# Optimization experiments

Hardware: AMD Instinct MI355X
Metric: run time of the kernel (lower is better)

Reference implementation:

```python
import jax, jax.numpy as jnp
import numpy as np

EMBED_SIZE = 1024
HEADS = 16
HEAD_DIM = EMBED_SIZE // HEADS
NEG_INF = -1e20


def setup_inputs() -> dict:
    key = jax.random.key(0)
    k1, k2, k3, k4, k5, k6, k7 = jax.random.split(key, 7)
    N, S = 2, 2048
    values = jax.random.normal(k1, (N, S, EMBED_SIZE), dtype=jnp.float32)
    keys = jax.random.normal(k2, (N, S, EMBED_SIZE), dtype=jnp.float32)
    query = jax.random.normal(k3, (N, S, EMBED_SIZE), dtype=jnp.float32)
    mask = jnp.ones((N, 1, S, S), dtype=bool)
    # Per-head projection weights (shared across heads), torch Linear convention y = x @ W.T
    sc = 1.0 / np.sqrt(HEAD_DIM)
    Wq = jax.random.uniform(k4, (HEAD_DIM, HEAD_DIM), jnp.float32, -sc, sc)
    Wk = jax.random.uniform(k5, (HEAD_DIM, HEAD_DIM), jnp.float32, -sc, sc)
    Wv = jax.random.uniform(k6, (HEAD_DIM, HEAD_DIM), jnp.float32, -sc, sc)
    sco = 1.0 / np.sqrt(EMBED_SIZE)
    k7a, k7b = jax.random.split(k7)
    Wo = jax.random.uniform(k7a, (EMBED_SIZE, EMBED_SIZE), jnp.float32, -sco, sco)
    bo = jax.random.uniform(k7b, (EMBED_SIZE,), jnp.float32, -sco, sco)
    return {"values": values, "keys": keys, "query": query, "mask": mask,
            "Wq": Wq, "Wk": Wk, "Wv": Wv, "Wo": Wo, "bo": bo}


def reference(values, keys, query, mask, Wq, Wk, Wv, Wo, bo):
    N, Q, E = query.shape
    K = keys.shape[1]
    H, D = HEADS, HEAD_DIM
    v = values.reshape(N, K, H, D)
    k = keys.reshape(N, K, H, D)
    q = query.reshape(N, Q, H, D)
    # per-head linear (weights shared across heads): y = x @ W.T
    q = jnp.einsum('nqhd,ed->nqhe', q, Wq)
    k = jnp.einsum('nkhd,ed->nkhe', k, Wk)
    v = jnp.einsum('nkhd,ed->nkhe', v, Wv)
    energy = jnp.einsum('nqhd,nkhd->nhqk', q, k)  # [N,H,Q,K]
    energy = jnp.where(mask, energy, NEG_INF)
    # NOTE: original scales by sqrt(embed_size), not sqrt(head_dim)
    attn = jax.nn.softmax(energy / (E ** 0.5), axis=-1)
    out = jnp.einsum('nhqk,nkhd->nqhd', attn, v).reshape(N, Q, H * D)
    return out @ Wo.T + bo
```

## Files before the change

kernel.cpp:

```cpp
#include <hip/hip_runtime.h>
#include <hip/hip_bf16.h>


typedef __bf16 bf16_t;
typedef __bf16 bf16x4_t __attribute__((ext_vector_type(4)));
typedef __bf16 bf16x8_t __attribute__((ext_vector_type(8)));
typedef float f32x4_t __attribute__((ext_vector_type(4)));

#define MFMA16(a, b, c) __builtin_amdgcn_mfma_f32_16x16x32_bf16((a), (b), (c), 0, 0, 0)

static __device__ __forceinline__ bf16x8_t cvt8(float4 a, float4 b) {
  bf16x8_t r = { (bf16_t)a.x, (bf16_t)a.y, (bf16_t)a.z, (bf16_t)a.w,
                 (bf16_t)b.x, (bf16_t)b.y, (bf16_t)b.z, (bf16_t)b.w };
  return r;
}

__global__ __launch_bounds__(256) void k_cvt_wo(const float* __restrict__ w,
                                                bf16_t* __restrict__ o) {
  int i = (blockIdx.x * 256 + threadIdx.x) * 4;
  float4 v = *(const float4*)(w + i);
  bf16x4_t r = { (bf16_t)v.x, (bf16_t)v.y, (bf16_t)v.z, (bf16_t)v.w };
  *(bf16x4_t*)(o + i) = r;
}

__global__ __launch_bounds__(256) void k_tilemask(const int* __restrict__ mask32,
                                                  unsigned char* __restrict__ tm) {
  const int b = blockIdx.x;
  const int n = b >> 10, qt = (b >> 5) & 31, kt = b & 31;
  const int t = threadIdx.x;
  const int row = t >> 2;
  const int mtype = (mask32[0] == 1);
  bool ok;
  if (mtype) {
    const uint4* base = (const uint4*)(mask32 + (size_t)n * 4194304 +
                                       (size_t)(qt * 64 + row) * 2048 + kt * 64);
    ok = true;
    #pragma unroll
    for (int j = 0; j < 4; ++j) {
      uint4 v = base[(t & 3) * 4 + j];
      ok = ok && v.x && v.y && v.z && v.w;
    }
  } else {
    const unsigned char* maskb = (const unsigned char*)mask32;
    const int c = (t & 3) * 16;
    uint4 v = *(const uint4*)(maskb + (size_t)n * 4194304 +
                              (size_t)(qt * 64 + row) * 2048 + kt * 64 + c);
    ok = ((v.x & v.y & v.z & v.w) == 0x01010101u);
  }
  __shared__ int ok_s;
  if (t == 0) ok_s = 1;
  __syncthreads();
  if (!ok) atomicAnd(&ok_s, 0);
  __syncthreads();
  if (t == 0) tm[b] = (unsigned char)ok_s;
}

__global__ __launch_bounds__(256) void k_proj_qk(const float* __restrict__ x,
                                                 const float* __restrict__ w,
                                                 bf16_t* __restrict__ out, float oscale) {
  __shared__ __align__(16) ushort Xs[256 * 64];
  const int t = threadIdx.x;
  const int r0 = blockIdx.x * 256;
  const int lane = t & 63, wv = t >> 6;
  const int g = lane >> 4, l15 = lane & 15;
  #pragma unroll
  for (int i = 0; i < 16; ++i) {
    int c = t + 256 * i;
    float4 v = *(const float4*)(x + (size_t)r0 * 64 + (size_t)c * 4);
    int row = c >> 4;
    int off = ((c & 15) * 8) ^ ((row & 7) << 4);
    bf16x4_t bv = { (bf16_t)v.x, (bf16_t)v.y, (bf16_t)v.z, (bf16_t)v.w };
    *(bf16x4_t*)((char*)Xs + row * 128 + off) = bv;
  }
  bf16x8_t bw[4][2];
  #pragma unroll
  for (int nf = 0; nf < 4; ++nf)
    #pragma unroll
    for (int ks = 0; ks < 2; ++ks) {
      const float* wp = w + (nf * 16 + l15) * 64 + ks * 32 + g * 8;
      bw[nf][ks] = cvt8(*(const float4*)wp, *(const float4*)(wp + 4));
    }
  __syncthreads();
  f32x4_t acc[4][4] = {};
  #pragma unroll
  for (int mi = 0; mi < 4; ++mi) {
    int row = wv * 64 + mi * 16 + l15;
    int sw = (row & 7) << 4;
    bf16x8_t a0 = *(const bf16x8_t*)((char*)Xs + row * 128 + ((g * 16) ^ sw));
    bf16x8_t a1 = *(const bf16x8_t*)((char*)Xs + row * 128 + ((64 + g * 16) ^ sw));
    #pragma unroll
    for (int nf = 0; nf < 4; ++nf) {
      acc[mi][nf] = MFMA16(a0, bw[nf][0], acc[mi][nf]);
      acc[mi][nf] = MFMA16(a1, bw[nf][1], acc[mi][nf]);
    }
  }
  #pragma unroll
  for (int mi = 0; mi < 4; ++mi)
    #pragma unroll
    for (int rr = 0; rr < 4; ++rr) {
      int r = r0 + wv * 64 + mi * 16 + g * 4 + rr;
      int h = r & 15, s = (r >> 4) & 2047, n = r >> 15;
      bf16_t* op = out + ((size_t)(n * 16 + h) * 2048 + s) * 64;
      #pragma unroll
      for (int nf = 0; nf < 4; ++nf)
        op[nf * 16 + l15] = (bf16_t)(acc[mi][nf][rr] * oscale);
    }
}

__global__ __launch_bounds__(256) void k_proj_v(const float* __restrict__ x,
                                                const float* __restrict__ w,
                                                bf16_t* __restrict__ vt) {
  const int b = blockIdx.x;
  const int sb = b & 7, nh = b >> 3;
  const int h = nh & 15, n = nh >> 4;
  const int t = threadIdx.x, lane = t & 63, wv = t >> 6;
  const int g = lane >> 4, l15 = lane & 15;
  const int s0 = sb * 256 + wv * 64;
  bf16x8_t bx[4][2];
  #pragma unroll
  for (int ni = 0; ni < 4; ++ni)
    #pragma unroll
    for (int ks = 0; ks < 2; ++ks) {
      int s = s0 + ni * 16 + l15;
      const float* xp = x + ((size_t)n * 2048 + s) * 1024 + h * 64 + ks * 32 + g * 8;
      bx[ni][ks] = cvt8(*(const float4*)xp, *(const float4*)(xp + 4));
    }
  f32x4_t acc[4][4] = {};
  #pragma unroll
  for (int mi = 0; mi < 4; ++mi) {
    const float* wp = w + (mi * 16 + l15) * 64 + g * 8;
    bf16x8_t a0 = cvt8(*(const float4*)wp, *(const float4*)(wp + 4));
    bf16x8_t a1 = cvt8(*(const float4*)(wp + 32), *(const float4*)(wp + 36));
    #pragma unroll
    for (int ni = 0; ni < 4; ++ni) {
      acc[mi][ni] = MFMA16(a0, bx[ni][0], acc[mi][ni]);
      acc[mi][ni] = MFMA16(a1, bx[ni][1], acc[mi][ni]);
    }
  }
  #pragma unroll
  for (int mi = 0; mi < 4; ++mi)
    #pragma unroll
    for (int rr = 0; rr < 4; ++rr) {
      int d = mi * 16 + g * 4 + rr;
      bf16_t* vp = vt + ((size_t)nh * 64 + d) * 2048 + s0;
      #pragma unroll
      for (int ni = 0; ni < 4; ++ni)
        vp[ni * 16 + l15] = (bf16_t)acc[mi][ni][rr];
    }
}

__global__ __launch_bounds__(256) void k_attn(const bf16_t* __restrict__ Qp,
                                              const bf16_t* __restrict__ Kp,
                                              const bf16_t* __restrict__ VT,
                                              const int* __restrict__ mask32,
                                              const unsigned char* __restrict__ tm,
                                              bf16_t* __restrict__ ao) {
  __shared__ __align__(16) ushort Ks[64 * 64];
  __shared__ __align__(16) ushort Vs[64 * 64];
  __shared__ __align__(16) ushort Ps[4 * 32 * 64];
  const int b = blockIdx.x;
  const int qb = b & 15, nh = b >> 4;
  const int n = nh >> 4, h = nh & 15;
  const int t = threadIdx.x, lane = t & 63, wv = t >> 6;
  const int g = lane >> 4, l15 = lane & 15;
  const int q0 = qb * 128 + wv * 32;
  const size_t kvbase = (size_t)nh * (2048 * 64);
  const int mtype = (mask32[0] == 1);

  bf16x8_t aq[2][2];
  #pragma unroll
  for (int mi = 0; mi < 2; ++mi)
    #pragma unroll
    for (int ks = 0; ks < 2; ++ks) {
      int qrow = q0 + mi * 16 + l15;
      aq[mi][ks] = *(const bf16x8_t*)(Qp + kvbase + (size_t)qrow * 64 + ks * 32 + g * 8);
    }

  f32x4_t o[2][4] = {};
  float mrow[2][4], lrow[2][4];
  #pragma unroll
  for (int mi = 0; mi < 2; ++mi)
    #pragma unroll
    for (int rr = 0; rr < 4; ++rr) { mrow[mi][rr] = -__builtin_inff(); lrow[mi][rr] = 0.f; }

  const unsigned char* tmrow = tm + ((size_t)n * 32 + (q0 >> 6)) * 32;
  const int srow = t >> 2, sc = t & 3;
  const int ssw = (srow & 7) << 4;

  for (int kt = 0; kt < 32; ++kt) {
    const int kb = kt * 64;
    {
      const float4* gk = (const float4*)(Kp + kvbase + (size_t)kb * 64);
      float4 k0 = gk[t * 2], k1 = gk[t * 2 + 1];
      *(float4*)((char*)Ks + srow * 128 + ((sc * 32) ^ ssw)) = k0;
      *(float4*)((char*)Ks + srow * 128 + ((sc * 32 + 16) ^ ssw)) = k1;
      const bf16_t* gv = VT + kvbase + (size_t)srow * 2048 + kb + sc * 16;
      float4 v0 = *(const float4*)gv, v1 = *(const float4*)(gv + 8);
      *(float4*)((char*)Vs + srow * 128 + ((sc * 32) ^ ssw)) = v0;
      *(float4*)((char*)Vs + srow * 128 + ((sc * 32 + 16) ^ ssw)) = v1;
    }
    __syncthreads();
    f32x4_t sfr[2][4] = {};
    #pragma unroll
    for (int ks = 0; ks < 2; ++ks)
      #pragma unroll
      for (int nf = 0; nf < 4; ++nf) {
        int kr = nf * 16 + l15;
        bf16x8_t kf = *(const bf16x8_t*)((char*)Ks + kr * 128 + ((ks * 64 + g * 16) ^ ((kr & 7) << 4)));
        sfr[0][nf] = MFMA16(aq[0][ks], kf, sfr[0][nf]);
        sfr[1][nf] = MFMA16(aq[1][ks], kf, sfr[1][nf]);
      }
    if (!tmrow[kt]) {
      #pragma unroll
      for (int mi = 0; mi < 2; ++mi)
        #pragma unroll
        for (int nf = 0; nf < 4; ++nf)
          #pragma unroll
          for (int rr = 0; rr < 4; ++rr) {
            int qrow = q0 + mi * 16 + g * 4 + rr;
            int kcol = kb + nf * 16 + l15;
            size_t mi_idx = (size_t)n * 4194304 + (size_t)qrow * 2048 + kcol;
            bool mv = mtype ? (mask32[mi_idx] != 0)
                            : (((const unsigned char*)mask32)[mi_idx] != 0);
            if (!mv) sfr[mi][nf][rr] = -3.125e18f;
          }
    }
    #pragma unroll
    for (int mi = 0; mi < 2; ++mi) {
      float al[4];
      #pragma unroll
      for (int rr = 0; rr < 4; ++rr) {
        float mx = fmaxf(fmaxf(sfr[mi][0][rr], sfr[mi][1][rr]),
                         fmaxf(sfr[mi][2][rr], sfr[mi][3][rr]));
        mx = fmaxf(mx, __shfl_xor(mx, 1));
        mx = fmaxf(mx, __shfl_xor(mx, 2));
        mx = fmaxf(mx, __shfl_xor(mx, 4));
        mx = fmaxf(mx, __shfl_xor(mx, 8));
        float mn = fmaxf(mrow[mi][rr], mx);
        al[rr] = __expf(mrow[mi][rr] - mn);
        mrow[mi][rr] = mn;
        float rs = 0.f;
        #pragma unroll
        for (int nf = 0; nf < 4; ++nf) {
          float p = __expf(sfr[mi][nf][rr] - mn);
          sfr[mi][nf][rr] = p;
          rs += p;
        }
        rs += __shfl_xor(rs, 1); rs += __shfl_xor(rs, 2);
        rs += __shfl_xor(rs, 4); rs += __shfl_xor(rs, 8);
        lrow[mi][rr] = lrow[mi][rr] * al[rr] + rs;
      }
      #pragma unroll
      for (int df = 0; df < 4; ++df)
        #pragma unroll
        for (int rr = 0; rr < 4; ++rr)
          o[mi][df][rr] *= al[rr];
      #pragma unroll
      for (int rr = 0; rr < 4; ++rr) {
        int prow = wv * 32 + mi * 16 + g * 4 + rr;
        char* pp = (char*)Ps + prow * 128;
        int sw = (prow & 7) << 4;
        #pragma unroll
        for (int nf = 0; nf < 4; ++nf)
          *(bf16_t*)(pp + (((nf * 16 + l15) * 2) ^ sw)) = (bf16_t)sfr[mi][nf][rr];
      }
    }
    asm volatile("" ::: "memory");
    #pragma unroll
    for (int ks = 0; ks < 2; ++ks) {
      bf16x8_t pa[2];
      #pragma unroll
      for (int mi = 0; mi < 2; ++mi) {
        int prow = wv * 32 + mi * 16 + l15;
        pa[mi] = *(const bf16x8_t*)((char*)Ps + prow * 128 + ((ks * 64 + g * 16) ^ ((prow & 7) << 4)));
      }
      #pragma unroll
      for (int df = 0; df < 4; ++df) {
        int vr = df * 16 + l15;
        bf16x8_t vf = *(const bf16x8_t*)((char*)Vs + vr * 128 + ((ks * 64 + g * 16) ^ ((vr & 7) << 4)));
        o[0][df] = MFMA16(pa[0], vf, o[0][df]);
        o[1][df] = MFMA16(pa[1], vf, o[1][df]);
      }
    }
    __syncthreads();
  }
  #pragma unroll
  for (int mi = 0; mi < 2; ++mi)
    #pragma unroll
    for (int rr = 0; rr < 4; ++rr) {
      float inv = 1.f / lrow[mi][rr];
      int qrow = q0 + mi * 16 + g * 4 + rr;
      bf16_t* op = ao + ((size_t)n * 2048 + qrow) * 1024 + h * 64;
      #pragma unroll
      for (int df = 0; df < 4; ++df)
        op[df * 16 + l15] = (bf16_t)(o[mi][df][rr] * inv);
    }
}

__global__ __launch_bounds__(256) void k_gemm_out(const bf16_t* __restrict__ A,
                                                  const bf16_t* __restrict__ B,
                                                  const float* __restrict__ bias,
                                                  float* __restrict__ C) {
  __shared__ __align__(16) ushort As[128 * 32];
  __shared__ __align__(16) ushort Bs[128 * 32];
  const int bx = blockIdx.x;
  const int mb = bx >> 3, nb = bx & 7;
  const int m0 = mb * 128, n0 = nb * 128;
  const int t = threadIdx.x, lane = t & 63, wv = t >> 6;
  const int g = lane >> 4, l15 = lane & 15;
  const int wm = (wv >> 1) * 64, wn = (wv & 1) * 64;
  const int srow = t >> 1, sc = (t & 1) * 16;
  f32x4_t acc[4][4] = {};
  for (int k0 = 0; k0 < 1024; k0 += 32) {
    float4 a0 = *(const float4*)(A + (size_t)(m0 + srow) * 1024 + k0 + sc);
    float4 a1 = *(const float4*)(A + (size_t)(m0 + srow) * 1024 + k0 + sc + 8);
    float4 b0 = *(const float4*)(B + (size_t)(n0 + srow) * 1024 + k0 + sc);
    float4 b1 = *(const float4*)(B + (size_t)(n0 + srow) * 1024 + k0 + sc + 8);
    *(float4*)((char*)As + srow * 64 + sc * 2) = a0;
    *(float4*)((char*)As + srow * 64 + sc * 2 + 16) = a1;
    *(float4*)((char*)Bs + srow * 64 + sc * 2) = b0;
    *(float4*)((char*)Bs + srow * 64 + sc * 2 + 16) = b1;
    __syncthreads();
    bf16x8_t af[4], bfr[4];
    #pragma unroll
    for (int mi = 0; mi < 4; ++mi)
      af[mi] = *(const bf16x8_t*)((char*)As + (wm + mi * 16 + l15) * 64 + g * 16);
    #pragma unroll
    for (int ni = 0; ni < 4; ++ni)
      bfr[ni] = *(const bf16x8_t*)((char*)Bs + (wn + ni * 16 + l15) * 64 + g * 16);
    #pragma unroll
    for (int mi = 0; mi < 4; ++mi)
      #pragma unroll
      for (int ni = 0; ni < 4; ++ni)
        acc[mi][ni] = MFMA16(af[mi], bfr[ni], acc[mi][ni]);
    __syncthreads();
  }
  float bv[4];
  #pragma unroll
  for (int ni = 0; ni < 4; ++ni) bv[ni] = bias[n0 + wn + ni * 16 + l15];
  #pragma unroll
  for (int mi = 0; mi < 4; ++mi)
    #pragma unroll
    for (int rr = 0; rr < 4; ++rr) {
      int row = m0 + wm + mi * 16 + g * 4 + rr;
      float* cp = C + (size_t)row * 1024 + n0 + wn;
      #pragma unroll
      for (int ni = 0; ni < 4; ++ni)
        cp[ni * 16 + l15] = acc[mi][ni][rr] + bv[ni];
    }
}

extern "C" void kernel_launch(void* const* d_in, const int* in_sizes, int n_in,
                              void* d_out, int out_size, void* d_ws, size_t ws_size,
                              hipStream_t stream) {
  (void)in_sizes; (void)n_in; (void)out_size; (void)ws_size;
  const float* values = (const float*)d_in[0];
  const float* keys   = (const float*)d_in[1];
  const float* query  = (const float*)d_in[2];
  const int*   mask   = (const int*)d_in[3];
  const float* Wq = (const float*)d_in[4];
  const float* Wk = (const float*)d_in[5];
  const float* Wv = (const float*)d_in[6];
  const float* Wo = (const float*)d_in[7];
  const float* bo = (const float*)d_in[8];
  float* out = (float*)d_out;

  char* ws = (char*)d_ws;
  bf16_t* Qp  = (bf16_t*)(ws);
  bf16_t* Kp  = (bf16_t*)(ws + (8u << 20));
  bf16_t* VTp = (bf16_t*)(ws + (16u << 20));
  bf16_t* AO  = (bf16_t*)(ws + (24u << 20));
  bf16_t* WOb = (bf16_t*)(ws + (32u << 20));
  unsigned char* TM = (unsigned char*)(ws + (34u << 20));

  k_cvt_wo<<<dim3(1024), dim3(256), 0, stream>>>(Wo, WOb);
  k_tilemask<<<dim3(2048), dim3(256), 0, stream>>>(mask, TM);
  k_proj_qk<<<dim3(256), dim3(256), 0, stream>>>(query, Wq, Qp, 0.03125f);
  k_proj_qk<<<dim3(256), dim3(256), 0, stream>>>(keys, Wk, Kp, 1.0f);
  k_proj_v<<<dim3(256), dim3(256), 0, stream>>>(values, Wv, VTp);
  k_attn<<<dim3(512), dim3(256), 0, stream>>>(Qp, Kp, VTp, mask, TM, AO);
  k_gemm_out<<<dim3(256), dim3(256), 0, stream>>>(AO, WOb, bo, out);
}
```

Baseline: 304.7 us.

## Rewrite attention kernel with 32x32 MFMA, transposed scores, and double-buffered LDS loads

The attention kernel now computes S^T with 32x32x16 MFMAs, so each lane owns one query row. That makes the row max and sum a single cross-half shuffle, and P can be rebuilt into the PV operand in registers instead of going through shared memory. K/V tiles are double-buffered and loaded straight into LDS with global_load_lds, overlapping the next tile's load with compute. Blocks grow to 512 threads covering 256 queries on half as many blocks, which may reduce parallelism across the GPU's CUs and raises register pressure.

```diff
diff --git a/kernel.cpp b/kernel.cpp
--- a/kernel.cpp
+++ b/kernel.cpp
@@ -6,13 +6,21 @@
 typedef __bf16 bf16x4_t __attribute__((ext_vector_type(4)));
 typedef __bf16 bf16x8_t __attribute__((ext_vector_type(8)));
 typedef float f32x4_t __attribute__((ext_vector_type(4)));
+typedef float f32x16_t __attribute__((ext_vector_type(16)));
 
 #define MFMA16(a, b, c) __builtin_amdgcn_mfma_f32_16x16x32_bf16((a), (b), (c), 0, 0, 0)
+#define MFMA32(a, b, c) __builtin_amdgcn_mfma_f32_32x32x16_bf16((a), (b), (c), 0, 0, 0)
 
 static __device__ __forceinline__ bf16x8_t cvt8(float4 a, float4 b) {
   bf16x8_t r = { (bf16_t)a.x, (bf16_t)a.y, (bf16_t)a.z, (bf16_t)a.w,
                  (bf16_t)b.x, (bf16_t)b.y, (bf16_t)b.z, (bf16_t)b.w };
   return r;
+}
+
+static __device__ __forceinline__ unsigned pack2(float a, float b) {
+  union { bf16_t h[2]; unsigned u; } x;
+  x.h[0] = (bf16_t)a; x.h[1] = (bf16_t)b;
+  return x.u;
 }
 
 __global__ __launch_bounds__(256) void k_cvt_wo(const float* __restrict__ w,
@@ -149,152 +157,157 @@
     }
 }
 
-__global__ __launch_bounds__(256) void k_attn(const bf16_t* __restrict__ Qp,
-                                              const bf16_t* __restrict__ Kp,
-                                              const bf16_t* __restrict__ VT,
-                                              const int* __restrict__ mask32,
-                                              const unsigned char* __restrict__ tm,
-                                              bf16_t* __restrict__ ao) {
-  __shared__ __align__(16) ushort Ks[64 * 64];
-  __shared__ __align__(16) ushort Vs[64 * 64];
-  __shared__ __align__(16) ushort Ps[4 * 32 * 64];
+__global__ __launch_bounds__(512, 2) void k_attn(const bf16_t* __restrict__ Qp,
+                                                 const bf16_t* __restrict__ Kp,
+                                                 const bf16_t* __restrict__ VT,
+                                                 const int* __restrict__ mask32,
+                                                 const unsigned char* __restrict__ tm,
+                                                 bf16_t* __restrict__ ao) {
+  __shared__ __align__(128) char lds[32768];
   const int b = blockIdx.x;
-  const int qb = b & 15, nh = b >> 4;
+  const int qb = b & 7, nh = b >> 3;
   const int n = nh >> 4, h = nh & 15;
   const int t = threadIdx.x, lane = t & 63, wv = t >> 6;
-  const int g = lane >> 4, l15 = lane & 15;
-  const int q0 = qb * 128 + wv * 32;
+  const int l31 = lane & 31, hi = lane >> 5;
+  const int q0w = qb * 256 + wv * 32;
   const size_t kvbase = (size_t)nh * (2048 * 64);
   const int mtype = (mask32[0] == 1);
 
-  bf16x8_t aq[2][2];
-  #pragma unroll
-  for (int mi = 0; mi < 2; ++mi)
-    #pragma unroll
-    for (int ks = 0; ks < 2; ++ks) {
-      int qrow = q0 + mi * 16 + l15;
-      aq[mi][ks] = *(const bf16x8_t*)(Qp + kvbase + (size_t)qrow * 64 + ks * 32 + g * 8);
-    }
-
-  f32x4_t o[2][4] = {};
-  float mrow[2][4], lrow[2][4];
-  #pragma unroll
-  for (int mi = 0; mi < 2; ++mi)
-    #pragma unroll
-    for (int rr = 0; rr < 4; ++rr) { mrow[mi][rr] = -__builtin_inff(); lrow[mi][rr] = 0.f; }
-
-  const unsigned char* tmrow = tm + ((size_t)n * 32 + (q0 >> 6)) * 32;
-  const int srow = t >> 2, sc = t & 3;
-  const int ssw = (srow & 7) << 4;
+  bf16x8_t qf[4];
+  #pragma unroll
+  for (int kd = 0; kd < 4; ++kd)
+    qf[kd] = *(const bf16x8_t*)(Qp + kvbase + (size_t)(q0w + l31) * 64 + kd * 16 + hi * 8);
+
+  f32x16_t o0 = {}, o1 = {};
+  float m_r = -3.0e38f, l_r = 0.f;
+
+  const unsigned char* tmrow = tm + ((size_t)n * 32 + (q0w >> 6)) * 32;
+
+  const int srow = lane >> 3, schunk = lane & 7;
+  const int soff = ((schunk << 4) ^ (srow << 4));
+  const char* gK = (const char*)(Kp + kvbase);
+  const char* gV = (const char*)(VT + kvbase);
+
+#define STAGE(ktile, bufsel)                                                          \
+  do {                                                                                \
+    const int kb_ = (ktile) * 64;                                                     \
+    char* ldsK_ = lds + (bufsel) * 16384 + wv * 1024;                                 \
+    char* ldsV_ = lds + (bufsel) * 16384 + 8192 + wv * 1024;                          \
+    __builtin_amdgcn_global_load_lds(                                                 \
+        (const __attribute__((address_space(1))) void*)(gK + (size_t)(kb_ + wv * 8 + srow) * 128 + soff), \
+        (__attribute__((address_space(3))) void*)ldsK_, 16, 0, 0);                    \
+    __builtin_amdgcn_global_load_lds(                                                 \
+        (const __attribute__((address_space(1))) void*)(gV + (size_t)(wv * 8 + srow) * 4096 + (size_t)kb_ * 2 + soff), \
+        (__attribute__((address_space(3))) void*)ldsV_, 16, 0, 0);                    \
+  } while (0)
+
+  int buf = 0;
+  STAGE(0, 0);
+  asm volatile("s_waitcnt vmcnt(0)" ::: "memory");
+  __syncthreads();
 
   for (int kt = 0; kt < 32; ++kt) {
-    const int kb = kt * 64;
-    {
-      const float4* gk = (const float4*)(Kp + kvbase + (size_t)kb * 64);
-      float4 k0 = gk[t * 2], k1 = gk[t * 2 + 1];
-      *(float4*)((char*)Ks + srow * 128 + ((sc * 32) ^ ssw)) = k0;
-      *(float4*)((char*)Ks + srow * 128 + ((sc * 32 + 16) ^ ssw)) = k1;
-      const bf16_t* gv = VT + kvbase + (size_t)srow * 2048 + kb + sc * 16;
-      float4 v0 = *(const float4*)gv, v1 = *(const float4*)(gv + 8);
-      *(float4*)((char*)Vs + srow * 128 + ((sc * 32) ^ ssw)) = v0;
-      *(float4*)((char*)Vs + srow * 128 + ((sc * 32 + 16) ^ ssw)) = v1;
-    }
+    if (kt < 31) STAGE(kt + 1, buf ^ 1);
+    const char* Ksb = lds + buf * 16384;
+    const char* Vsb = Ksb + 8192;
+    const int rsw = (l31 & 7) << 4;
+
+    f32x16_t s0 = {}, s1 = {};
+    #pragma unroll
+    for (int kd = 0; kd < 4; ++kd) {
+      int off = kd * 32 + hi * 16;
+      bf16x8_t k0 = *(const bf16x8_t*)(Ksb + l31 * 128 + (off ^ rsw));
+      bf16x8_t k1 = *(const bf16x8_t*)(Ksb + (32 + l31) * 128 + (off ^ rsw));
+      s0 = MFMA32(k0, qf[kd], s0);
+      s1 = MFMA32(k1, qf[kd], s1);
+    }
+
+    if (!tmrow[kt]) {
+      #pragma unroll
+      for (int r = 0; r < 16; ++r) {
+        int krow = (r & 3) + 8 * (r >> 2) + 4 * hi;
+        size_t base = (size_t)n * 4194304 + (size_t)(q0w + l31) * 2048 + kt * 64 + krow;
+        bool m0 = mtype ? (mask32[base] != 0) : (((const unsigned char*)mask32)[base] != 0);
+        bool m1 = mtype ? (mask32[base + 32] != 0) : (((const unsigned char*)mask32)[base + 32] != 0);
+        if (!m0) s0[r] = -3.125e18f;
+        if (!m1) s1[r] = -3.125e18f;
+      }
+    }
+
+    float mx = s0[0];
+    #pragma unroll
+    for (int r = 1; r < 16; ++r) mx = fmaxf(mx, s0[r]);
+    #pragma unroll
+    for (int r = 0; r < 16; ++r) mx = fmaxf(mx, s1[r]);
+    mx = fmaxf(mx, __shfl_xor(mx, 32));
+    float mn = fmaxf(m_r, mx);
+    float alpha = __expf(m_r - mn);
+    m_r = mn;
+    float rs = 0.f;
+    #pragma unroll
+    for (int r = 0; r < 16; ++r) { float p = __expf(s0[r] - mn); s0[r] = p; rs += p; }
+    #pragma unroll
+    for (int r = 0; r < 16; ++r) { float p = __expf(s1[r] - mn); s1[r] = p; rs += p; }
+    rs += __shfl_xor(rs, 32);
+    l_r = l_r * alpha + rs;
+    o0 *= alpha;
+    o1 *= alpha;
+
+    unsigned pk0[4][2], pk1[4][2];
+    #pragma unroll
+    for (int rq = 0; rq < 4; ++rq)
+      #pragma unroll
+      for (int w = 0; w < 2; ++w) {
+        pk0[rq][w] = pack2(s0[4 * rq + 2 * w], s0[4 * rq + 2 * w + 1]);
+        pk1[rq][w] = pack2(s1[4 * rq + 2 * w], s1[4 * rq + 2 * w + 1]);
+      }
+    bf16x8_t paf[4];
+    #pragma unroll
+    for (int tt = 0; tt < 2; ++tt)
+      #pragma unroll
+      for (int k2 = 0; k2 < 2; ++k2) {
+        unsigned a0 = tt ? pk1[2 * k2][0] : pk0[2 * k2][0];
+        unsigned a1 = tt ? pk1[2 * k2][1] : pk0[2 * k2][1];
+        unsigned b0 = tt ? pk1[2 * k2 + 1][0] : pk0[2 * k2 + 1][0];
+        unsigned b1 = tt ? pk1[2 * k2 + 1][1] : pk0[2 * k2 + 1][1];
+        unsigned sa0 = __shfl_xor(a0, 32), sa1 = __shfl_xor(a1, 32);
+        unsigned sb0 = __shfl_xor(b0, 32), sb1 = __shfl_xor(b1, 32);
+        union { unsigned u[4]; bf16x8_t v; } f;
+        f.u[0] = hi ? sb0 : a0;
+        f.u[1] = hi ? sb1 : a1;
+        f.u[2] = hi ? b0 : sa0;
+        f.u[3] = hi ? b1 : sa1;
+        paf[tt * 2 + k2] = f.v;
+      }
+
+    #pragma unroll
+    for (int ks = 0; ks < 4; ++ks) {
+      int off = ks * 32 + hi * 16;
+      bf16x8_t v0 = *(const bf16x8_t*)(Vsb + l31 * 128 + (off ^ rsw));
+      bf16x8_t v1 = *(const bf16x8_t*)(Vsb + (32 + l31) * 128 + (off ^ rsw));
+      o0 = MFMA32(v0, paf[ks], o0);
+      o1 = MFMA32(v1, paf[ks], o1);
+    }
+
+    asm volatile("s_waitcnt vmcnt(0)" ::: "memory");
     __syncthreads();
-    f32x4_t sfr[2][4] = {};
-    #pragma unroll
-    for (int ks = 0; ks < 2; ++ks)
-      #pragma unroll
-      for (int nf = 0; nf < 4; ++nf) {
-        int kr = nf * 16 + l15;
-        bf16x8_t kf = *(const bf16x8_t*)((char*)Ks + kr * 128 + ((ks * 64 + g * 16) ^ ((kr & 7) << 4)));
-        sfr[0][nf] = MFMA16(aq[0][ks], kf, sfr[0][nf]);
-        sfr[1][nf] = MFMA16(aq[1][ks], kf, sfr[1][nf]);
-      }
-    if (!tmrow[kt]) {
-      #pragma unroll
-      for (int mi = 0; mi < 2; ++mi)
-        #pragma unroll
-        for (int nf = 0; nf < 4; ++nf)
-          #pragma unroll
-          for (int rr = 0; rr < 4; ++rr) {
-            int qrow = q0 + mi * 16 + g * 4 + rr;
-            int kcol = kb + nf * 16 + l15;
-            size_t mi_idx = (size_t)n * 4194304 + (size_t)qrow * 2048 + kcol;
-            bool mv = mtype ? (mask32[mi_idx] != 0)
-                            : (((const unsigned char*)mask32)[mi_idx] != 0);
-            if (!mv) sfr[mi][nf][rr] = -3.125e18f;
-          }
-    }
-    #pragma unroll
-    for (int mi = 0; mi < 2; ++mi) {
-      float al[4];
-      #pragma unroll
-      for (int rr = 0; rr < 4; ++rr) {
-        float mx = fmaxf(fmaxf(sfr[mi][0][rr], sfr[mi][1][rr]),
-                         fmaxf(sfr[mi][2][rr], sfr[mi][3][rr]));
-        mx = fmaxf(mx, __shfl_xor(mx, 1));
-        mx = fmaxf(mx, __shfl_xor(mx, 2));
-        mx = fmaxf(mx, __shfl_xor(mx, 4));
-        mx = fmaxf(mx, __shfl_xor(mx, 8));
-        float mn = fmaxf(mrow[mi][rr], mx);
-        al[rr] = __expf(mrow[mi][rr] - mn);
-        mrow[mi][rr] = mn;
-        float rs = 0.f;
-        #pragma unroll
-        for (int nf = 0; nf < 4; ++nf) {
-          float p = __expf(sfr[mi][nf][rr] - mn);
-          sfr[mi][nf][rr] = p;
-          rs += p;
-        }
-        rs += __shfl_xor(rs, 1); rs += __shfl_xor(rs, 2);
-        rs += __shfl_xor(rs, 4); rs += __shfl_xor(rs, 8);
-        lrow[mi][rr] = lrow[mi][rr] * al[rr] + rs;
-      }
-      #pragma unroll
-      for (int df = 0; df < 4; ++df)
-        #pragma unroll
-        for (int rr = 0; rr < 4; ++rr)
-          o[mi][df][rr] *= al[rr];
-      #pragma unroll
-      for (int rr = 0; rr < 4; ++rr) {
-        int prow = wv * 32 + mi * 16 + g * 4 + rr;
-        char* pp = (char*)Ps + prow * 128;
-        int sw = (prow & 7) << 4;
-        #pragma unroll
-        for (int nf = 0; nf < 4; ++nf)
-          *(bf16_t*)(pp + (((nf * 16 + l15) * 2) ^ sw)) = (bf16_t)sfr[mi][nf][rr];
-      }
-    }
-    asm volatile("" ::: "memory");
-    #pragma unroll
-    for (int ks = 0; ks < 2; ++ks) {
-      bf16x8_t pa[2];
-      #pragma unroll
-      for (int mi = 0; mi < 2; ++mi) {
-        int prow = wv * 32 + mi * 16 + l15;
-        pa[mi] = *(const bf16x8_t*)((char*)Ps + prow * 128 + ((ks * 64 + g * 16) ^ ((prow & 7) << 4)));
-      }
-      #pragma unroll
-      for (int df = 0; df < 4; ++df) {
-        int vr = df * 16 + l15;
-        bf16x8_t vf = *(const bf16x8_t*)((char*)Vs + vr * 128 + ((ks * 64 + g * 16) ^ ((vr & 7) << 4)));
-        o[0][df] = MFMA16(pa[0], vf, o[0][df]);
-        o[1][df] = MFMA16(pa[1], vf, o[1][df]);
-      }
-    }
-    __syncthreads();
-  }
-  #pragma unroll
-  for (int mi = 0; mi < 2; ++mi)
-    #pragma unroll
-    for (int rr = 0; rr < 4; ++rr) {
-      float inv = 1.f / lrow[mi][rr];
-      int qrow = q0 + mi * 16 + g * 4 + rr;
-      bf16_t* op = ao + ((size_t)n * 2048 + qrow) * 1024 + h * 64;
-      #pragma unroll
-      for (int df = 0; df < 4; ++df)
-        op[df * 16 + l15] = (bf16_t)(o[mi][df][rr] * inv);
-    }
+    buf ^= 1;
+  }
+#undef STAGE
+
+  float inv = 1.f / l_r;
+  bf16_t* op = ao + ((size_t)n * 2048 + q0w + l31) * 1024 + h * 64;
+  #pragma unroll
+  for (int rq = 0; rq < 4; ++rq) {
+    bf16x4_t w0, w1;
+    #pragma unroll
+    for (int e = 0; e < 4; ++e) {
+      w0[e] = (bf16_t)(o0[4 * rq + e] * inv);
+      w1[e] = (bf16_t)(o1[4 * rq + e] * inv);
+    }
+    *(bf16x4_t*)(op + 8 * rq + 4 * hi) = w0;
+    *(bf16x4_t*)(op + 32 + 8 * rq + 4 * hi) = w1;
+  }
 }
 
 __global__ __launch_bounds__(256) void k_gemm_out(const bf16_t* __restrict__ A,
@@ -378,6 +391,6 @@
   k_proj_qk<<<dim3(256), dim3(256), 0, stream>>>(query, Wq, Qp, 0.03125f);
   k_proj_qk<<<dim3(256), dim3(256), 0, stream>>>(keys, Wk, Kp, 1.0f);
   k_proj_v<<<dim3(256), dim3(256), 0, stream>>>(values, Wv, VTp);
-  k_attn<<<dim3(512), dim3(256), 0, stream>>>(Qp, Kp, VTp, mask, TM, AO);
+  k_attn<<<dim3(256), dim3(512), 0, stream>>>(Qp, Kp, VTp, mask, TM, AO);
   k_gemm_out<<<dim3(256), dim3(256), 0, stream>>>(AO, WOb, bo, out);
 }
```

After: 260.1 us. 14.6% less time.
